# Kernel optimization log

Hardware: AMD Instinct MI355X
Metric: run time of the kernel (lower is better)

Reference implementation:

```python
import jax, jax.numpy as jnp
import numpy as np

INPUT_DIM = 1024
OUTPUT_DIM = 1024


def setup_inputs() -> dict:
    key = jax.random.key(0)
    k1, k2, k3, k4 = jax.random.split(key, 4)
    B, S, D = 4, 2048, INPUT_DIM
    src = jax.random.normal(k1, (B, S, D), dtype=jnp.float32)
    tgt = jax.random.normal(k2, (B, S, D), dtype=jnp.float32)
    # nn.Linear(input_dim*2, output_dim): weight [out, in], bias [out]
    bound = 1.0 / np.sqrt(2 * D)
    W = jax.random.uniform(k3, (OUTPUT_DIM, 2 * D), jnp.float32, -bound, bound)
    b = jax.random.uniform(k4, (OUTPUT_DIM,), jnp.float32, -bound, bound)
    return {"src": src, "tgt": tgt, "W": W, "b": b}


def reference(src, tgt, W, b):
    # weight = bmm(tgt, src^T): [B, S_tgt, S_src]
    weight = jnp.einsum("btd,bsd->bts", tgt, src)
    # NOTE: original uses Softmax(dim=1) -> normalizes over the tgt axis
    weight = jax.nn.softmax(weight, axis=1)
    # weighted sum over src positions: [B, S_tgt, D]
    weight_sum = jnp.einsum("bts,bsd->btd", weight, src)
    output = jnp.concatenate([weight_sum, tgt], axis=2)  # [B, S_tgt, 2D]
    output = output @ W.T + b  # [B, S_tgt, output_dim]
    return (output, weight)
```

## Files before the change

### kernel.cpp

```cpp
#include <hip/hip_runtime.h>
#include <stdint.h>


#define B_   4
#define S_   2048
#define D_   1024
#define OUTD 1024

typedef unsigned short ushort_t;
typedef _Float16 half8 __attribute__((ext_vector_type(8)));
typedef float    f32x4 __attribute__((ext_vector_type(4)));

__device__ __forceinline__ ushort_t f2h(float f) {
    union { _Float16 h; ushort_t u; } v;
    v.h = (_Float16)f;
    return v.u;
}
__device__ __forceinline__ float h2f(ushort_t u) {
    union { _Float16 h; ushort_t u; } v;
    v.u = u;
    return (float)v.h;
}

__device__ __forceinline__ void ld16(const ushort_t* g, ushort_t* l) {
    __builtin_amdgcn_global_load_lds(
        (const __attribute__((address_space(1))) void*)g,
        (__attribute__((address_space(3))) void*)l, 16, 0, 0);
}


__global__ void k_split(const float4* __restrict__ src, const float4* __restrict__ tgt,
                        ushort4* __restrict__ sh,
                        ushort4* __restrict__ th, ushort4* __restrict__ tl)
{
    const int64_t n4 = (int64_t)B_ * S_ * D_ / 4;
    for (int64_t i = (int64_t)blockIdx.x * blockDim.x + threadIdx.x; i < n4;
         i += (int64_t)gridDim.x * blockDim.x) {
        float4 s = src[i];
        sh[i] = (ushort4){f2h(s.x), f2h(s.y), f2h(s.z), f2h(s.w)};
        float4 tv = tgt[i];
        ushort4 ht = {f2h(tv.x), f2h(tv.y), f2h(tv.z), f2h(tv.w)};
        th[i] = ht;
        tl[i] = (ushort4){f2h(tv.x - h2f(ht.x)), f2h(tv.y - h2f(ht.y)),
                          f2h(tv.z - h2f(ht.z)), f2h(tv.w - h2f(ht.w))};
    }
}

__global__ void k_wconv(const float4* __restrict__ W, ushort4* __restrict__ wb)
{
    const int64_t n4 = (int64_t)OUTD * 2 * D_ / 4;
    for (int64_t i = (int64_t)blockIdx.x * blockDim.x + threadIdx.x; i < n4;
         i += (int64_t)gridDim.x * blockDim.x) {
        float4 w = W[i];
        wb[i] = (ushort4){f2h(w.x), f2h(w.y), f2h(w.z), f2h(w.w)};
    }
}

__launch_bounds__(256)
__global__ void k_gemm_logits(const ushort_t* __restrict__ Ah, const ushort_t* __restrict__ Al,
                              const ushort_t* __restrict__ Bs,
                              float* __restrict__ C,
                              float* __restrict__ pm, float* __restrict__ ps)
{
    const int M = S_, N = S_, K = D_;
    int b = blockIdx.z;
    Ah += (int64_t)b * M * K;  Al += (int64_t)b * M * K;
    Bs += (int64_t)b * N * K;
    C  += (int64_t)b * M * N;

    __shared__ __align__(16) ushort_t sAh[128 * 32], sAl[128 * 32], sB[128 * 32];
    __shared__ float red_m[2][128], red_s[2][128];

    int t    = threadIdx.x;
    int m0   = blockIdx.y * 128, n0 = blockIdx.x * 128;
    int wave = t >> 6, lane = t & 63;
    int wr   = (wave >> 1) * 64, wc = (wave & 1) * 64;
    int l15  = lane & 15, quad = lane >> 4;

    f32x4 acc[4][4];
#pragma unroll
    for (int i = 0; i < 4; i++)
#pragma unroll
        for (int j = 0; j < 4; j++) acc[i][j] = (f32x4){0.f, 0.f, 0.f, 0.f};

    int srow = t >> 2;
    int scol = (t & 3) * 8;

    const ushort_t* gAh0 = Ah + (int64_t)(m0 + srow) * K + scol;
    const ushort_t* gAh1 = gAh0 + (int64_t)64 * K;
    const ushort_t* gAl0 = Al + (int64_t)(m0 + srow) * K + scol;
    const ushort_t* gAl1 = gAl0 + (int64_t)64 * K;
    const ushort_t* gB0  = Bs + (int64_t)(n0 + srow) * K + scol;
    const ushort_t* gB1  = gB0 + (int64_t)64 * K;

    ushort_t* lAh0 = sAh + wave * 512;  ushort_t* lAh1 = sAh + 2048 + wave * 512;
    ushort_t* lAl0 = sAl + wave * 512;  ushort_t* lAl1 = sAl + 2048 + wave * 512;
    ushort_t* lB0  = sB  + wave * 512;  ushort_t* lB1  = sB  + 2048 + wave * 512;

    for (int k0 = 0; k0 < K; k0 += 32) {
        ld16(gAh0, lAh0);  ld16(gAh1, lAh1);
        ld16(gAl0, lAl0);  ld16(gAl1, lAl1);
        ld16(gB0,  lB0);   ld16(gB1,  lB1);
        gAh0 += 32; gAh1 += 32; gAl0 += 32; gAl1 += 32; gB0 += 32; gB1 += 32;
        __syncthreads();

        half8 ah[4], al[4], bf[4];
#pragma unroll
        for (int i = 0; i < 4; i++) {
            ah[i] = *(const half8*)(&sAh[(wr + i * 16 + l15) * 32 + quad * 8]);
            al[i] = *(const half8*)(&sAl[(wr + i * 16 + l15) * 32 + quad * 8]);
        }
#pragma unroll
        for (int j = 0; j < 4; j++)
            bf[j] = *(const half8*)(&sB[(wc + j * 16 + l15) * 32 + quad * 8]);
#pragma unroll
        for (int i = 0; i < 4; i++)
#pragma unroll
            for (int j = 0; j < 4; j++) {
                acc[i][j] = __builtin_amdgcn_mfma_f32_16x16x32_f16(ah[i], bf[j], acc[i][j], 0, 0, 0);
                acc[i][j] = __builtin_amdgcn_mfma_f32_16x16x32_f16(al[i], bf[j], acc[i][j], 0, 0, 0);
            }
        __syncthreads();
    }

#pragma unroll
    for (int i = 0; i < 4; i++) {
        int row_base = m0 + wr + i * 16 + quad * 4;
#pragma unroll
        for (int j = 0; j < 4; j++) {
            int col = n0 + wc + j * 16 + l15;
#pragma unroll
            for (int r = 0; r < 4; r++)
                C[(int64_t)(row_base + r) * N + col] = acc[i][j][r];
        }
    }

    int rowhalf = wave >> 1;
#pragma unroll
    for (int j = 0; j < 4; j++) {
        float m = -3.0e38f;
#pragma unroll
        for (int i = 0; i < 4; i++)
#pragma unroll
            for (int r = 0; r < 4; r++) m = fmaxf(m, acc[i][j][r]);
        float s = 0.f;
#pragma unroll
        for (int i = 0; i < 4; i++)
#pragma unroll
            for (int r = 0; r < 4; r++) s += __expf(acc[i][j][r] - m);
#pragma unroll
        for (int d = 16; d <= 32; d <<= 1) {
            float m2 = __shfl_xor(m, d, 64);
            float s2 = __shfl_xor(s, d, 64);
            float nm = fmaxf(m, m2);
            s = s * __expf(m - nm) + s2 * __expf(m2 - nm);
            m = nm;
        }
        if (lane < 16) {
            red_m[rowhalf][wc + j * 16 + l15] = m;
            red_s[rowhalf][wc + j * 16 + l15] = s;
        }
    }
    __syncthreads();
    if (t < 128) {
        float ma = red_m[0][t], mb = red_m[1][t];
        float sa = red_s[0][t], sb = red_s[1][t];
        float m = fmaxf(ma, mb);
        float s = sa * __expf(ma - m) + sb * __expf(mb - m);
        int idx = blockIdx.y * (B_ * S_) + b * S_ + n0 + t;
        pm[idx] = m;
        ps[idx] = s;
    }
}


__global__ void k_colstats2(const float* __restrict__ pm, const float* __restrict__ ps,
                            float* __restrict__ cmax, float* __restrict__ cinv)
{
    int i = blockIdx.x * 256 + threadIdx.x;
    float m = -3.0e38f;
#pragma unroll
    for (int c = 0; c < 16; c++) m = fmaxf(m, pm[c * (B_ * S_) + i]);
    float sum = 0.f;
#pragma unroll
    for (int c = 0; c < 16; c++) sum += ps[c * (B_ * S_) + i] * __expf(pm[c * (B_ * S_) + i] - m);
    cmax[i] = m;
    cinv[i] = 1.0f / sum;
}

__global__ void k_softmax_norm(float4* __restrict__ L, const float4* __restrict__ cmax4,
                               const float4* __restrict__ cinv4, ushort4* __restrict__ wbf)
{
    const int64_t n4 = (int64_t)B_ * S_ * S_ / 4;
    for (int64_t i = (int64_t)blockIdx.x * blockDim.x + threadIdx.x; i < n4;
         i += (int64_t)gridDim.x * blockDim.x) {
        int b  = (int)(i >> 20);
        int c4 = (int)(i & 511);
        float4 x  = L[i];
        float4 cm = cmax4[b * 512 + c4];
        float4 ci = cinv4[b * 512 + c4];
        float4 w;
        w.x = __expf(x.x - cm.x) * ci.x;
        w.y = __expf(x.y - cm.y) * ci.y;
        w.z = __expf(x.z - cm.z) * ci.z;
        w.w = __expf(x.w - cm.w) * ci.w;
        L[i] = w;
        wbf[i] = (ushort4){f2h(w.x), f2h(w.y), f2h(w.z), f2h(w.w)};
    }
}

__launch_bounds__(256)
__global__ void k_gemm_nt_f16(const ushort_t* __restrict__ A, int lda, int64_t bsA,
                              const ushort_t* __restrict__ Bm, int ldb, int64_t bsB,
                              ushort_t* __restrict__ C, int ldc, int64_t bsC, int K)
{
    int b = blockIdx.z;
    A  += (int64_t)b * bsA;
    Bm += (int64_t)b * bsB;
    C  += (int64_t)b * bsC;

    __shared__ __align__(16) ushort_t sA[128 * 64], sB[128 * 64];

    int t    = threadIdx.x;
    int m0   = blockIdx.y * 128, n0 = blockIdx.x * 128;
    int wave = t >> 6, lane = t & 63;
    int wr   = (wave >> 1) * 64, wc = (wave & 1) * 64;
    int l15  = lane & 15, quad = lane >> 4;
    int e7   = l15 & 7;

    f32x4 acc[4][4];
#pragma unroll
    for (int i = 0; i < 4; i++)
#pragma unroll
        for (int j = 0; j < 4; j++) acc[i][j] = (f32x4){0.f, 0.f, 0.f, 0.f};

    int srow = t >> 3;
    int scol = (((t & 7) ^ (srow & 7)) * 8);

    const ushort_t* gA = A  + (int64_t)(m0 + srow) * lda + scol;
    const ushort_t* gB = Bm + (int64_t)(n0 + srow) * ldb + scol;
    ushort_t* lA = sA + wave * 512;
    ushort_t* lB = sB + wave * 512;

    for (int k0 = 0; k0 < K; k0 += 64) {
#pragma unroll
        for (int j = 0; j < 4; j++) {
            ld16(gA + (int64_t)(j * 32) * lda + k0, lA + j * 2048);
            ld16(gB + (int64_t)(j * 32) * ldb + k0, lB + j * 2048);
        }
        __syncthreads();
#pragma unroll
        for (int ks = 0; ks < 64; ks += 32) {
            int gchunk = (ks >> 3) + quad;
            int slot   = (gchunk ^ e7) * 8;
            half8 af[4], bf[4];
#pragma unroll
            for (int i = 0; i < 4; i++)
                af[i] = *(const half8*)(&sA[(wr + i * 16 + l15) * 64 + slot]);
#pragma unroll
            for (int j = 0; j < 4; j++)
                bf[j] = *(const half8*)(&sB[(wc + j * 16 + l15) * 64 + slot]);
#pragma unroll
            for (int i = 0; i < 4; i++)
#pragma unroll
                for (int j = 0; j < 4; j++)
                    acc[i][j] = __builtin_amdgcn_mfma_f32_16x16x32_f16(af[i], bf[j], acc[i][j], 0, 0, 0);
        }
        __syncthreads();
    }

#pragma unroll
    for (int i = 0; i < 4; i++) {
        int row_base = m0 + wr + i * 16 + quad * 4;
#pragma unroll
        for (int j = 0; j < 4; j++) {
            int col = n0 + wc + j * 16 + l15;
#pragma unroll
            for (int r = 0; r < 4; r++)
                C[(int64_t)(row_base + r) * ldc + col] = f2h(acc[i][j][r]);
        }
    }
}

__launch_bounds__(256)
__global__ void k_gemm_final(const ushort_t* __restrict__ Wt, const ushort_t* __restrict__ PT,
                             const ushort_t* __restrict__ Q, const float* __restrict__ bias,
                             float* __restrict__ out)
{
    const int K = S_, N = OUTD;
    int b = blockIdx.z;
    const ushort_t* A  = Wt + (int64_t)b * S_ * S_;
    const ushort_t* Bm = PT + (int64_t)b * OUTD * S_;
    const ushort_t* Qb = Q  + (int64_t)b * S_ * OUTD;
    float* Cb = out + (int64_t)b * S_ * OUTD;

    __shared__ __align__(16) ushort_t sA[128 * 64], sB[128 * 64];

    int t    = threadIdx.x;
    int m0   = blockIdx.y * 128, n0 = blockIdx.x * 128;
    int wave = t >> 6, lane = t & 63;
    int wr   = (wave >> 1) * 64, wc = (wave & 1) * 64;
    int l15  = lane & 15, quad = lane >> 4;
    int e7   = l15 & 7;

    f32x4 acc[4][4];
#pragma unroll
    for (int i = 0; i < 4; i++)
#pragma unroll
        for (int j = 0; j < 4; j++) acc[i][j] = (f32x4){0.f, 0.f, 0.f, 0.f};

    int srow = t >> 3;
    int scol = (((t & 7) ^ (srow & 7)) * 8);

    const ushort_t* gA = A  + (int64_t)(m0 + srow) * K + scol;
    const ushort_t* gB = Bm + (int64_t)(n0 + srow) * K + scol;
    ushort_t* lA = sA + wave * 512;
    ushort_t* lB = sB + wave * 512;

    for (int k0 = 0; k0 < K; k0 += 64) {
#pragma unroll
        for (int j = 0; j < 4; j++) {
            ld16(gA + (int64_t)(j * 32) * K + k0, lA + j * 2048);
            ld16(gB + (int64_t)(j * 32) * K + k0, lB + j * 2048);
        }
        __syncthreads();
#pragma unroll
        for (int ks = 0; ks < 64; ks += 32) {
            int gchunk = (ks >> 3) + quad;
            int slot   = (gchunk ^ e7) * 8;
            half8 af[4], bf[4];
#pragma unroll
            for (int i = 0; i < 4; i++)
                af[i] = *(const half8*)(&sA[(wr + i * 16 + l15) * 64 + slot]);
#pragma unroll
            for (int j = 0; j < 4; j++)
                bf[j] = *(const half8*)(&sB[(wc + j * 16 + l15) * 64 + slot]);
#pragma unroll
            for (int i = 0; i < 4; i++)
#pragma unroll
                for (int j = 0; j < 4; j++)
                    acc[i][j] = __builtin_amdgcn_mfma_f32_16x16x32_f16(af[i], bf[j], acc[i][j], 0, 0, 0);
        }
        __syncthreads();
    }

#pragma unroll
    for (int i = 0; i < 4; i++) {
        int row_base = m0 + wr + i * 16 + quad * 4;
#pragma unroll
        for (int j = 0; j < 4; j++) {
            int col = n0 + wc + j * 16 + l15;
            float bv = bias[col];
#pragma unroll
            for (int r = 0; r < 4; r++) {
                int64_t idx = (int64_t)(row_base + r) * N + col;
                Cb[idx] = acc[i][j][r] + h2f(Qb[idx]) + bv;
            }
        }
    }
}


extern "C" void kernel_launch(void* const* d_in, const int* in_sizes, int n_in,
                              void* d_out, int out_size, void* d_ws, size_t ws_size,
                              hipStream_t stream)
{
    const float* src  = (const float*)d_in[0];
    const float* tgt  = (const float*)d_in[1];
    const float* W    = (const float*)d_in[2];
    const float* bias = (const float*)d_in[3];

    float* out = (float*)d_out;
    float* Lw  = out + (size_t)B_ * S_ * OUTD;

    char*  ws = (char*)d_ws;
    size_t o  = 0;
    auto take = [&](size_t bytes) -> char* {
        char* p = ws + o;
        o += (bytes + 255) & ~(size_t)255;
        return p;
    };
    const size_t ELEMS = (size_t)B_ * S_ * D_;
    ushort_t* sh   = (ushort_t*)take(ELEMS * 2);
    ushort_t* th   = (ushort_t*)take(ELEMS * 2);
    ushort_t* tl   = (ushort_t*)take(ELEMS * 2);
    ushort_t* wbf  = (ushort_t*)take((size_t)B_ * S_ * S_ * 2);
    ushort_t* wb   = (ushort_t*)take((size_t)OUTD * 2 * D_ * 2);
    ushort_t* PT   = (ushort_t*)take((size_t)B_ * OUTD * S_ * 2);
    ushort_t* Qb   = (ushort_t*)take((size_t)B_ * S_ * OUTD * 2);
    float*    pm   = (float*)take(16 * (size_t)B_ * S_ * 4);
    float*    ps   = (float*)take(16 * (size_t)B_ * S_ * 4);
    float*    cmax = (float*)take((size_t)B_ * S_ * 4);
    float*    cinv = (float*)take((size_t)B_ * S_ * 4);
    (void)ws_size; (void)in_sizes; (void)n_in; (void)out_size;

    k_split<<<dim3(2048), dim3(256), 0, stream>>>((const float4*)src, (const float4*)tgt,
                                                  (ushort4*)sh, (ushort4*)th, (ushort4*)tl);
    k_wconv<<<dim3(512), dim3(256), 0, stream>>>((const float4*)W, (ushort4*)wb);

    k_gemm_nt_f16<<<dim3(16, 8, 4), dim3(256), 0, stream>>>(
        wb, 2 * D_, 0,
        sh, D_, (int64_t)S_ * D_,
        PT, S_, (int64_t)OUTD * S_, D_);

    k_gemm_nt_f16<<<dim3(8, 16, 4), dim3(256), 0, stream>>>(
        th, D_, (int64_t)S_ * D_,
        wb + D_, 2 * D_, 0,
        Qb, OUTD, (int64_t)S_ * OUTD, D_);

    k_gemm_logits<<<dim3(16, 16, 4), dim3(256), 0, stream>>>(th, tl, sh, Lw, pm, ps);

    k_colstats2<<<dim3(32), dim3(256), 0, stream>>>(pm, ps, cmax, cinv);
    k_softmax_norm<<<dim3(2048), dim3(256), 0, stream>>>((float4*)Lw, (const float4*)cmax,
                                                         (const float4*)cinv, (ushort4*)wbf);

    k_gemm_final<<<dim3(8, 16, 4), dim3(256), 0, stream>>>(wbf, PT, Qb, bias, out);
}
```

Before: 374.9 us.

## Merge logits and projection GEMMs into one launch; deepen K tile in final GEMM

Combines the two projection GEMMs (W·src^T and tgt·W2^T) and the logits GEMM into a single kernel whose blocks alternate between logits tiles and projection tiles. The aim is to remove launch gaps and tail underutilisation between the independent GEMMs and let them share the machine concurrently. Separately, the final GEMM now loads a 128-wide K tile per iteration with a 16-way XOR swizzle, halving the number of barrier-separated iterations. The trade-off is larger shared memory use (64KB in the final GEMM, 32KB plus reductions in the merged kernel), which may reduce occupancy, and the mixed kernel takes on the register pressure of the heavier logits path.

```diff
diff --git a/kernel.cpp b/kernel.cpp
--- a/kernel.cpp
+++ b/kernel.cpp
@@ -56,23 +56,92 @@
     }
 }
 
-__launch_bounds__(256)
-__global__ void k_gemm_logits(const ushort_t* __restrict__ Ah, const ushort_t* __restrict__ Al,
-                              const ushort_t* __restrict__ Bs,
-                              float* __restrict__ C,
-                              float* __restrict__ pm, float* __restrict__ ps)
+
+__device__ __forceinline__ void nt_body(ushort_t* smem, int t, int bx, int by,
+                                        const ushort_t* __restrict__ A, int lda,
+                                        const ushort_t* __restrict__ Bm, int ldb,
+                                        ushort_t* __restrict__ C, int ldc, int K)
+{
+    ushort_t* sA = smem;
+    ushort_t* sB = smem + 8192;
+
+    int m0   = by * 128, n0 = bx * 128;
+    int wave = t >> 6, lane = t & 63;
+    int wr   = (wave >> 1) * 64, wc = (wave & 1) * 64;
+    int l15  = lane & 15, quad = lane >> 4;
+    int e7   = l15 & 7;
+
+    f32x4 acc[4][4];
+#pragma unroll
+    for (int i = 0; i < 4; i++)
+#pragma unroll
+        for (int j = 0; j < 4; j++) acc[i][j] = (f32x4){0.f, 0.f, 0.f, 0.f};
+
+    int srow = t >> 3;
+    int scol = (((t & 7) ^ (srow & 7)) * 8);
+
+    const ushort_t* gA = A  + (int64_t)(m0 + srow) * lda + scol;
+    const ushort_t* gB = Bm + (int64_t)(n0 + srow) * ldb + scol;
+    ushort_t* lA = sA + wave * 512;
+    ushort_t* lB = sB + wave * 512;
+
+    for (int k0 = 0; k0 < K; k0 += 64) {
+#pragma unroll
+        for (int j = 0; j < 4; j++) {
+            ld16(gA + (int64_t)(j * 32) * lda + k0, lA + j * 2048);
+            ld16(gB + (int64_t)(j * 32) * ldb + k0, lB + j * 2048);
+        }
+        __syncthreads();
+#pragma unroll
+        for (int ks = 0; ks < 64; ks += 32) {
+            int slot = (((ks >> 3) + quad) ^ e7) * 8;
+            half8 af[4], bf[4];
+#pragma unroll
+            for (int i = 0; i < 4; i++)
+                af[i] = *(const half8*)(&sA[(wr + i * 16 + l15) * 64 + slot]);
+#pragma unroll
+            for (int j = 0; j < 4; j++)
+                bf[j] = *(const half8*)(&sB[(wc + j * 16 + l15) * 64 + slot]);
+#pragma unroll
+            for (int i = 0; i < 4; i++)
+#pragma unroll
+                for (int j = 0; j < 4; j++)
+                    acc[i][j] = __builtin_amdgcn_mfma_f32_16x16x32_f16(af[i], bf[j], acc[i][j], 0, 0, 0);
+        }
+        __syncthreads();
+    }
+
+#pragma unroll
+    for (int i = 0; i < 4; i++) {
+        int row_base = m0 + wr + i * 16 + quad * 4;
+#pragma unroll
+        for (int j = 0; j < 4; j++) {
+            int col = n0 + wc + j * 16 + l15;
+#pragma unroll
+            for (int r = 0; r < 4; r++)
+                C[(int64_t)(row_base + r) * ldc + col] = f2h(acc[i][j][r]);
+        }
+    }
+}
+
+__device__ __forceinline__ void logits_body(ushort_t* smem, float (*red_m)[128], float (*red_s)[128],
+                                            int t, int bx, int by, int b,
+                                            const ushort_t* __restrict__ Ah,
+                                            const ushort_t* __restrict__ Al,
+                                            const ushort_t* __restrict__ Bs,
+                                            float* __restrict__ C,
+                                            float* __restrict__ pm, float* __restrict__ ps)
 {
     const int M = S_, N = S_, K = D_;
-    int b = blockIdx.z;
     Ah += (int64_t)b * M * K;  Al += (int64_t)b * M * K;
     Bs += (int64_t)b * N * K;
     C  += (int64_t)b * M * N;
 
-    __shared__ __align__(16) ushort_t sAh[128 * 32], sAl[128 * 32], sB[128 * 32];
-    __shared__ float red_m[2][128], red_s[2][128];
-
-    int t    = threadIdx.x;
-    int m0   = blockIdx.y * 128, n0 = blockIdx.x * 128;
+    ushort_t* sAh = smem;
+    ushort_t* sAl = smem + 4096;
+    ushort_t* sB  = smem + 8192;
+
+    int m0   = by * 128, n0 = bx * 128;
     int wave = t >> 6, lane = t & 63;
     int wr   = (wave >> 1) * 64, wc = (wave & 1) * 64;
     int l15  = lane & 15, quad = lane >> 4;
@@ -167,9 +236,44 @@
         float sa = red_s[0][t], sb = red_s[1][t];
         float m = fmaxf(ma, mb);
         float s = sa * __expf(ma - m) + sb * __expf(mb - m);
-        int idx = blockIdx.y * (B_ * S_) + b * S_ + n0 + t;
+        int idx = by * (B_ * S_) + b * S_ + n0 + t;
         pm[idx] = m;
         ps[idx] = s;
+    }
+}
+
+__launch_bounds__(256)
+__global__ void k_mega(const ushort_t* __restrict__ sh, const ushort_t* __restrict__ th,
+                       const ushort_t* __restrict__ tl, const ushort_t* __restrict__ wb,
+                       ushort_t* __restrict__ PT, ushort_t* __restrict__ Qb,
+                       float* __restrict__ C, float* __restrict__ pm, float* __restrict__ ps)
+{
+    __shared__ __align__(16) ushort_t smem[16384];
+    __shared__ float red_m[2][128], red_s[2][128];
+
+    int id = blockIdx.x;
+    int t  = threadIdx.x;
+
+    if ((id & 1) == 0) {
+        int lid = id >> 1;
+        int bx = lid & 15, by = (lid >> 4) & 15, bz = lid >> 8;
+        logits_body(smem, red_m, red_s, t, bx, by, bz, th, tl, sh, C, pm, ps);
+    } else {
+        int oid = id >> 1;
+        if (oid < 512) {
+            int bx = oid & 15, by = (oid >> 4) & 7, bz = oid >> 7;
+            nt_body(smem, t, bx, by,
+                    wb, 2 * D_,
+                    sh + (int64_t)bz * S_ * D_, D_,
+                    PT + (int64_t)bz * OUTD * S_, S_, D_);
+        } else {
+            int qid = oid - 512;
+            int bx = qid & 7, by = (qid >> 3) & 15, bz = qid >> 7;
+            nt_body(smem, t, bx, by,
+                    th + (int64_t)bz * S_ * D_, D_,
+                    wb + D_, 2 * D_,
+                    Qb + (int64_t)bz * S_ * OUTD, OUTD, D_);
+        }
     }
 }
 
@@ -210,79 +314,6 @@
 }
 
 __launch_bounds__(256)
-__global__ void k_gemm_nt_f16(const ushort_t* __restrict__ A, int lda, int64_t bsA,
-                              const ushort_t* __restrict__ Bm, int ldb, int64_t bsB,
-                              ushort_t* __restrict__ C, int ldc, int64_t bsC, int K)
-{
-    int b = blockIdx.z;
-    A  += (int64_t)b * bsA;
-    Bm += (int64_t)b * bsB;
-    C  += (int64_t)b * bsC;
-
-    __shared__ __align__(16) ushort_t sA[128 * 64], sB[128 * 64];
-
-    int t    = threadIdx.x;
-    int m0   = blockIdx.y * 128, n0 = blockIdx.x * 128;
-    int wave = t >> 6, lane = t & 63;
-    int wr   = (wave >> 1) * 64, wc = (wave & 1) * 64;
-    int l15  = lane & 15, quad = lane >> 4;
-    int e7   = l15 & 7;
-
-    f32x4 acc[4][4];
-#pragma unroll
-    for (int i = 0; i < 4; i++)
-#pragma unroll
-        for (int j = 0; j < 4; j++) acc[i][j] = (f32x4){0.f, 0.f, 0.f, 0.f};
-
-    int srow = t >> 3;
-    int scol = (((t & 7) ^ (srow & 7)) * 8);
-
-    const ushort_t* gA = A  + (int64_t)(m0 + srow) * lda + scol;
-    const ushort_t* gB = Bm + (int64_t)(n0 + srow) * ldb + scol;
-    ushort_t* lA = sA + wave * 512;
-    ushort_t* lB = sB + wave * 512;
-
-    for (int k0 = 0; k0 < K; k0 += 64) {
-#pragma unroll
-        for (int j = 0; j < 4; j++) {
-            ld16(gA + (int64_t)(j * 32) * lda + k0, lA + j * 2048);
-            ld16(gB + (int64_t)(j * 32) * ldb + k0, lB + j * 2048);
-        }
-        __syncthreads();
-#pragma unroll
-        for (int ks = 0; ks < 64; ks += 32) {
-            int gchunk = (ks >> 3) + quad;
-            int slot   = (gchunk ^ e7) * 8;
-            half8 af[4], bf[4];
-#pragma unroll
-            for (int i = 0; i < 4; i++)
-                af[i] = *(const half8*)(&sA[(wr + i * 16 + l15) * 64 + slot]);
-#pragma unroll
-            for (int j = 0; j < 4; j++)
-                bf[j] = *(const half8*)(&sB[(wc + j * 16 + l15) * 64 + slot]);
-#pragma unroll
-            for (int i = 0; i < 4; i++)
-#pragma unroll
-                for (int j = 0; j < 4; j++)
-                    acc[i][j] = __builtin_amdgcn_mfma_f32_16x16x32_f16(af[i], bf[j], acc[i][j], 0, 0, 0);
-        }
-        __syncthreads();
-    }
-
-#pragma unroll
-    for (int i = 0; i < 4; i++) {
-        int row_base = m0 + wr + i * 16 + quad * 4;
-#pragma unroll
-        for (int j = 0; j < 4; j++) {
-            int col = n0 + wc + j * 16 + l15;
-#pragma unroll
-            for (int r = 0; r < 4; r++)
-                C[(int64_t)(row_base + r) * ldc + col] = f2h(acc[i][j][r]);
-        }
-    }
-}
-
-__launch_bounds__(256)
 __global__ void k_gemm_final(const ushort_t* __restrict__ Wt, const ushort_t* __restrict__ PT,
                              const ushort_t* __restrict__ Q, const float* __restrict__ bias,
                              float* __restrict__ out)
@@ -294,14 +325,13 @@
     const ushort_t* Qb = Q  + (int64_t)b * S_ * OUTD;
     float* Cb = out + (int64_t)b * S_ * OUTD;
 
-    __shared__ __align__(16) ushort_t sA[128 * 64], sB[128 * 64];
+    __shared__ __align__(16) ushort_t sA[128 * 128], sB[128 * 128];
 
     int t    = threadIdx.x;
     int m0   = blockIdx.y * 128, n0 = blockIdx.x * 128;
     int wave = t >> 6, lane = t & 63;
     int wr   = (wave >> 1) * 64, wc = (wave & 1) * 64;
     int l15  = lane & 15, quad = lane >> 4;
-    int e7   = l15 & 7;
 
     f32x4 acc[4][4];
 #pragma unroll
@@ -309,32 +339,31 @@
 #pragma unroll
         for (int j = 0; j < 4; j++) acc[i][j] = (f32x4){0.f, 0.f, 0.f, 0.f};
 
-    int srow = t >> 3;
-    int scol = (((t & 7) ^ (srow & 7)) * 8);
+    int srow = t >> 4;
+    int scol = ((t & 15) ^ srow) * 8;
 
     const ushort_t* gA = A  + (int64_t)(m0 + srow) * K + scol;
     const ushort_t* gB = Bm + (int64_t)(n0 + srow) * K + scol;
     ushort_t* lA = sA + wave * 512;
     ushort_t* lB = sB + wave * 512;
 
-    for (int k0 = 0; k0 < K; k0 += 64) {
-#pragma unroll
-        for (int j = 0; j < 4; j++) {
-            ld16(gA + (int64_t)(j * 32) * K + k0, lA + j * 2048);
-            ld16(gB + (int64_t)(j * 32) * K + k0, lB + j * 2048);
-        }
-        __syncthreads();
-#pragma unroll
-        for (int ks = 0; ks < 64; ks += 32) {
-            int gchunk = (ks >> 3) + quad;
-            int slot   = (gchunk ^ e7) * 8;
+    for (int k0 = 0; k0 < K; k0 += 128) {
+#pragma unroll
+        for (int p = 0; p < 8; p++) {
+            ld16(gA + (int64_t)(p * 16) * K + k0, lA + p * 2048);
+            ld16(gB + (int64_t)(p * 16) * K + k0, lB + p * 2048);
+        }
+        __syncthreads();
+#pragma unroll
+        for (int ks = 0; ks < 128; ks += 32) {
+            int slot = (((ks >> 3) + quad) ^ l15) * 8;
             half8 af[4], bf[4];
 #pragma unroll
             for (int i = 0; i < 4; i++)
-                af[i] = *(const half8*)(&sA[(wr + i * 16 + l15) * 64 + slot]);
+                af[i] = *(const half8*)(&sA[(wr + i * 16 + l15) * 128 + slot]);
 #pragma unroll
             for (int j = 0; j < 4; j++)
-                bf[j] = *(const half8*)(&sB[(wc + j * 16 + l15) * 64 + slot]);
+                bf[j] = *(const half8*)(&sB[(wc + j * 16 + l15) * 128 + slot]);
 #pragma unroll
             for (int i = 0; i < 4; i++)
 #pragma unroll
@@ -398,17 +427,7 @@
                                                   (ushort4*)sh, (ushort4*)th, (ushort4*)tl);
     k_wconv<<<dim3(512), dim3(256), 0, stream>>>((const float4*)W, (ushort4*)wb);
 
-    k_gemm_nt_f16<<<dim3(16, 8, 4), dim3(256), 0, stream>>>(
-        wb, 2 * D_, 0,
-        sh, D_, (int64_t)S_ * D_,
-        PT, S_, (int64_t)OUTD * S_, D_);
-
-    k_gemm_nt_f16<<<dim3(8, 16, 4), dim3(256), 0, stream>>>(
-        th, D_, (int64_t)S_ * D_,
-        wb + D_, 2 * D_, 0,
-        Qb, OUTD, (int64_t)S_ * OUTD, D_);
-
-    k_gemm_logits<<<dim3(16, 16, 4), dim3(256), 0, stream>>>(th, tl, sh, Lw, pm, ps);
+    k_mega<<<dim3(2048), dim3(256), 0, stream>>>(sh, th, tl, wb, PT, Qb, Lw, pm, ps);
 
     k_colstats2<<<dim3(32), dim3(256), 0, stream>>>(pm, ps, cmax, cinv);
     k_softmax_norm<<<dim3(2048), dim3(256), 0, stream>>>((float4*)Lw, (const float4*)cmax,
```

Measured after the change: 381.8 us. Within noise of the previous version (+1.8%).
